# Performance work log

Hardware: AMD Instinct MI355X
Metric: run time of the kernel (lower is better)

## Reference

```python
import jax, jax.numpy as jnp
import numpy as np

B, T, C, HR = 8, 4096, 256, 4
N_LAYER, LAYER_ID = 12, 3
HID = HR * C


def _fancy_decay_first():
    # Faithful reproduction of VRWKV_SpatialMix._init_weights(init_mode='fancy')
    r01 = LAYER_ID / (N_LAYER - 1)
    h = np.arange(C, dtype=np.float32)
    decay = -5.0 + 8.0 * (h / (C - 1)) ** (0.7 + 1.3 * r01)
    zig = ((np.arange(1, C + 1) % 3) - 1).astype(np.float32) * 0.5
    first = np.float32(np.log(0.3)) + zig
    return jnp.asarray(decay, jnp.float32), jnp.asarray(first, jnp.float32)


def setup_inputs() -> dict:
    key = jax.random.key(0)
    ks = jax.random.split(key, 12)
    s = 0.02  # small weight scale keeps exp(k) well-conditioned
    decay, first = _fancy_decay_first()
    return {
        "x": jax.random.normal(ks[0], (B, T, C), jnp.float32),
        "Wk": jax.random.normal(ks[1], (C, C), jnp.float32) * s,
        "Wv": jax.random.normal(ks[2], (C, C), jnp.float32) * s,
        "Wr": jax.random.normal(ks[3], (C, C), jnp.float32) * s,
        "Wo": jax.random.normal(ks[4], (C, C), jnp.float32) * s,
        "Wk_ffn": jax.random.normal(ks[5], (C, HID), jnp.float32) * s,
        "Wv_ffn": jax.random.normal(ks[6], (HID, C), jnp.float32) * s,
        "Wr_ffn": jax.random.normal(ks[7], (C, C), jnp.float32) * s,
        "g1": 1.0 + 0.1 * jax.random.normal(ks[8], (C,), jnp.float32),
        "b1": 0.1 * jax.random.normal(ks[9], (C,), jnp.float32),
        "g2": 1.0 + 0.1 * jax.random.normal(ks[10], (C,), jnp.float32),
        "b2": 0.1 * jax.random.normal(ks[11], (C,), jnp.float32),
        "spatial_decay": decay,
        "spatial_first": first,
    }


def _ln(x, g, b):
    m = jnp.mean(x, axis=-1, keepdims=True)
    v = jnp.var(x, axis=-1, keepdims=True)
    return (x - m) * jax.lax.rsqrt(v + 1e-5) * g + b


def _wkv(w, u, k, v):
    # Numerically-stable log-space WKV recurrence (same math as wkv_cuda):
    # y_t = (sum_{i<t} e^{w*(t-1-i)+k_i} v_i + e^{u+k_t} v_t)
    #     / (sum_{i<t} e^{w*(t-1-i)+k_i}     + e^{u+k_t})
    # w,u: [C]; k,v: [B,T,C] -> y: [B,T,C]
    Bb, Tt, Cc = k.shape
    kT = jnp.swapaxes(k, 0, 1)  # [T,B,C]
    vT = jnp.swapaxes(v, 0, 1)

    def step(carry, kv):
        p, q, o = carry           # [B,C] num / den / running max exponent
        kt, vt = kv               # [B,C]
        no = jnp.maximum(o, u + kt)
        A = jnp.exp(o - no)
        E = jnp.exp(u + kt - no)
        y = (A * p + E * vt) / (A * q + E)
        no2 = jnp.maximum(w + o, kt)
        A2 = jnp.exp(w + o - no2)
        E2 = jnp.exp(kt - no2)
        return (A2 * p + E2 * vt, A2 * q + E2, no2), y

    init = (jnp.zeros((Bb, Cc), k.dtype),
            jnp.zeros((Bb, Cc), k.dtype),
            jnp.full((Bb, Cc), -1e38, k.dtype))
    _, yT = jax.lax.scan(step, init, (kT, vT))
    return jnp.swapaxes(yT, 0, 1)


def reference(x, Wk, Wv, Wr, Wo, Wk_ffn, Wv_ffn, Wr_ffn, g1, b1, g2, b2,
              spatial_decay, spatial_first):
    Tlen = x.shape[1]
    # --- SpatialMix (shift_pixel=0 -> xk=xv=xr=h, key_norm=False) ---
    h = _ln(x, g1, b1)
    k = h @ Wk
    v = h @ Wv
    sr = jax.nn.sigmoid(h @ Wr)
    y = _wkv(spatial_decay / Tlen, spatial_first / Tlen, k, v)
    x = x + (sr * y) @ Wo
    # --- ChannelMix (square-ReLU MLP, sigmoid receptance gate) ---
    h2 = _ln(x, g2, b2)
    kk = jnp.square(jax.nn.relu(h2 @ Wk_ffn))
    x = x + jax.nn.sigmoid(h2 @ Wr_ffn) * (kk @ Wv_ffn)
    return x
```

## Files before the change

### kernel.cpp

```cpp
#include <hip/hip_runtime.h>
#include <hip/hip_bf16.h>
#include <math.h>

#define TDIM 4096
#define CDIM 256
#define BDIM 8
#define NTOK (BDIM * TDIM)
#define HIDDIM 1024
#define NCHUNK 256
#define CHLEN 16

typedef float f32x4 __attribute__((ext_vector_type(4)));
typedef __bf16 bf16x8 __attribute__((ext_vector_type(8)));
typedef __bf16 bf16x4 __attribute__((ext_vector_type(4)));
typedef long long i64x2 __attribute__((ext_vector_type(2)));

#define GLDS16(gp, lp) __builtin_amdgcn_global_load_lds( \
    (const __attribute__((address_space(1))) void*)(gp), \
    (__attribute__((address_space(3))) void*)(lp), 16, 0, 0)

#define WAITCNT_VM8  0x0F78
#define WAITCNT_VM5  0x0F75
#define WAITCNT_VM4  0x0F74
#define WAITCNT_VM0  0x0F70

__device__ __forceinline__ float sigm(float v) { return 1.0f / (1.0f + __expf(-v)); }

__device__ __forceinline__ int permk(int k) {
  return (k & ~63) + (((k >> 3) & 3) << 4) + (((k >> 5) & 1) << 3) + (k & 7);
}

__global__ __launch_bounds__(256) void pack_weights(
    const float* __restrict__ Wk, const float* __restrict__ Wv,
    const float* __restrict__ Wr, const float* __restrict__ Wo,
    const float* __restrict__ Wkf, const float* __restrict__ Wvf,
    const float* __restrict__ Wrf,
    __bf16* __restrict__ WoT, unsigned char* __restrict__ Wkvr8,
    unsigned char* __restrict__ Wkfr8, unsigned char* __restrict__ Wvf8) {
  long long j = (long long)blockIdx.x * 256 + threadIdx.x;
  if (j < 49152) {
    const long long d = j * 4;
    const int n = (int)(d >> 8), k0 = (int)(d & 255);
    const float* src = (n < 256) ? Wk : (n < 512 ? Wv : Wr);
    const int nn = n & 255;
    int w = 0;
    w = __builtin_amdgcn_cvt_pk_fp8_f32(src[k0 * 256 + nn],
                                        src[(k0 + 1) * 256 + nn], w, false);
    w = __builtin_amdgcn_cvt_pk_fp8_f32(src[(k0 + 2) * 256 + nn],
                                        src[(k0 + 3) * 256 + nn], w, true);
    *(int*)&Wkvr8[(long long)n * 256 + permk(k0)] = w;
    return;
  }
  j -= 49152;
  if (j < 65536) { int n = (int)(j >> 8), k = (int)(j & 255);
    WoT[j] = (__bf16)Wo[k * 256 + n]; return; }
  j -= 65536;
  if (j < 81920) {
    const long long d = j * 4;
    const int n = (int)(d >> 8), k0 = (int)(d & 255);
    float v0, v1, v2, v3;
    if (n < 1024) {
      v0 = Wkf[(long long)k0 * 1024 + n];       v1 = Wkf[(long long)(k0 + 1) * 1024 + n];
      v2 = Wkf[(long long)(k0 + 2) * 1024 + n]; v3 = Wkf[(long long)(k0 + 3) * 1024 + n];
    } else {
      const int m = n - 1024;
      v0 = Wrf[k0 * 256 + m];       v1 = Wrf[(k0 + 1) * 256 + m];
      v2 = Wrf[(k0 + 2) * 256 + m]; v3 = Wrf[(k0 + 3) * 256 + m];
    }
    int w = 0;
    w = __builtin_amdgcn_cvt_pk_fp8_f32(v0, v1, w, false);
    w = __builtin_amdgcn_cvt_pk_fp8_f32(v2, v3, w, true);
    *(int*)&Wkfr8[(long long)n * 256 + permk(k0)] = w;
    return;
  }
  j -= 81920;
  if (j < 65536) {
    const long long d = j * 4;
    const int n = (int)(d >> 10), k0 = (int)(d & 1023);
    int w = 0;
    w = __builtin_amdgcn_cvt_pk_fp8_f32(Wvf[(long long)k0 * 256 + n],
                                        Wvf[(long long)(k0 + 1) * 256 + n], w, false);
    w = __builtin_amdgcn_cvt_pk_fp8_f32(Wvf[(long long)(k0 + 2) * 256 + n],
                                        Wvf[(long long)(k0 + 3) * 256 + n], w, true);
    *(int*)&Wvf8[(long long)n * 1024 + permk(k0)] = w;
    return;
  }
}

__global__ __launch_bounds__(256) void ln_kernel(
    const float* __restrict__ x, const float* __restrict__ gamma,
    const float* __restrict__ beta, unsigned char* __restrict__ h8) {
  const int wave = threadIdx.x >> 6, lane = threadIdx.x & 63;
  const long long row = (long long)blockIdx.x * 4 + wave;
  const long long base = row * CDIM + lane * 4;
  const f32x4 v = *(const f32x4*)&x[base];
  float s = v[0] + v[1] + v[2] + v[3];
  float s2 = v[0]*v[0] + v[1]*v[1] + v[2]*v[2] + v[3]*v[3];
  #pragma unroll
  for (int o = 1; o < 64; o <<= 1) { s += __shfl_xor(s, o); s2 += __shfl_xor(s2, o); }
  const float mean = s * (1.0f / CDIM);
  const float var = s2 * (1.0f / CDIM) - mean * mean;
  const float rstd = rsqrtf(var + 1e-5f);
  const f32x4 g4 = *(const f32x4*)&gamma[lane * 4];
  const f32x4 b4 = *(const f32x4*)&beta[lane * 4];
  float o0 = (v[0] - mean) * rstd * g4[0] + b4[0];
  float o1 = (v[1] - mean) * rstd * g4[1] + b4[1];
  float o2 = (v[2] - mean) * rstd * g4[2] + b4[2];
  float o3 = (v[3] - mean) * rstd * g4[3] + b4[3];
  int w = 0;
  w = __builtin_amdgcn_cvt_pk_fp8_f32(o0, o1, w, false);
  w = __builtin_amdgcn_cvt_pk_fp8_f32(o2, o3, w, true);
  *(int*)&h8[row * CDIM + permk(lane * 4)] = w;
}

template <int EPI, int NY>
__global__ __launch_bounds__(512, 4) void gemmF(
    const unsigned char* __restrict__ A8, const unsigned char* __restrict__ B8,
    __bf16* __restrict__ outH, __bf16* __restrict__ outH2,
    unsigned char* __restrict__ outC) {
  constexpr int NTILES = 256 * NY;
  constexpr int TPB = NTILES / 512;
  static_assert(NTILES % 512 == 0, "grid divisibility");
  __shared__ unsigned char sA[2][4 * 8192];

  const int tid = threadIdx.x;
  const int wave = tid >> 6, lane = tid & 63;
  const int quad = lane >> 4, mrow = lane & 15;
  const int wm = (wave & 1) * 64, wn = (wave >> 1) * 32;
  const int srow = lane >> 2;
  const int o16 = (lane & 3) * 16;
  const int t0 = blockIdx.x * TPB;

  auto issueA = [&](int t, int buf) {
    const long long bm = (long long)(t & 255) * 128;
    const int r0 = wave * 16;
    #pragma unroll
    for (int g = 0; g < 4; g++)
      GLDS16(A8 + (bm + r0 + srow) * 256 + g * 64 + o16,
             &sA[buf][g * 8192 + r0 * 64]);
  };

  i64x2 fb[2][4];
  auto loadB = [&](int y) {
    const long long bn = (long long)y * 128;
    #pragma unroll
    for (int nt = 0; nt < 2; nt++)
      #pragma unroll
      for (int g = 0; g < 4; g++)
        fb[nt][g] = *(const i64x2*)
            &B8[(bn + wn + nt * 16 + mrow) * 256 + g * 64 + quad * 16];
  };

  issueA(t0, 0);
  int prevy = -1;

  #pragma unroll 1
  for (int i = 0; i < TPB; i++) {
    const int t = t0 + i;
    const int y = t >> 8;
    const bool ych = (y != prevy);
    prevy = y;

    if (i == 0) __builtin_amdgcn_s_waitcnt(WAITCNT_VM0);
    else        __builtin_amdgcn_s_waitcnt(WAITCNT_VM8);
    __builtin_amdgcn_s_barrier();

    if (ych) loadB(y);
    if (i + 1 < TPB) issueA(t + 1, (i + 1) & 1);
    if (ych) __builtin_amdgcn_s_waitcnt(WAITCNT_VM8);

    f32x4 acc[4][2] = {};
    const int buf = i & 1;
    #pragma unroll
    for (int g = 0; g < 4; g++) {
      i64x2 fa[4];
      #pragma unroll
      for (int mt = 0; mt < 4; mt++)
        fa[mt] = *(const i64x2*)
            &sA[buf][g * 8192 + (wm + mt * 16 + mrow) * 64 + quad * 16];
      #pragma unroll
      for (int c = 0; c < 2; c++)
        #pragma unroll
        for (int mt = 0; mt < 4; mt++)
          #pragma unroll
          for (int nt = 0; nt < 2; nt++)
            acc[mt][nt] = __builtin_amdgcn_mfma_f32_16x16x32_fp8_fp8(
                fb[nt][g][c], fa[mt][c], acc[mt][nt], 0, 0, 0);
    }

    const long long bm = (long long)(t & 255) * 128;
    if (EPI == 0) {
      const int plane = y >> 1;
      __bf16* o = outH + (long long)plane * (32768LL * 256);
      const int cb = (y & 1) * 128 + wn + quad * 4;
      #pragma unroll
      for (int mt = 0; mt < 4; mt++) {
        const long long row = bm + wm + mt * 16 + mrow;
        #pragma unroll
        for (int nt = 0; nt < 2; nt++) {
          const f32x4 a = acc[mt][nt];
          bf16x4 v;
          if (plane == 2) {
            #pragma unroll
            for (int r = 0; r < 4; r++) v[r] = (__bf16)sigm(a[r]);
          } else {
            #pragma unroll
            for (int r = 0; r < 4; r++) v[r] = (__bf16)a[r];
          }
          *(bf16x4*)&o[row * 256 + cb + nt * 16] = v;
        }
      }
    } else {
      if (y < 8) {
        const int cb = y * 128 + wn + quad * 4;
        #pragma unroll
        for (int mt = 0; mt < 4; mt++) {
          const long long row = bm + wm + mt * 16 + mrow;
          #pragma unroll
          for (int nt = 0; nt < 2; nt++) {
            const f32x4 a = acc[mt][nt];
            float q0 = a[0] > 0.0f ? a[0] : 0.0f;
            float q1 = a[1] > 0.0f ? a[1] : 0.0f;
            float q2 = a[2] > 0.0f ? a[2] : 0.0f;
            float q3 = a[3] > 0.0f ? a[3] : 0.0f;
            int w = 0;
            w = __builtin_amdgcn_cvt_pk_fp8_f32(q0 * q0, q1 * q1, w, false);
            w = __builtin_amdgcn_cvt_pk_fp8_f32(q2 * q2, q3 * q3, w, true);
            *(int*)&outC[row * 1024 + permk(cb + nt * 16)] = w;
          }
        }
      } else {
        const int cb = (y - 8) * 128 + wn + quad * 4;
        #pragma unroll
        for (int mt = 0; mt < 4; mt++) {
          const long long row = bm + wm + mt * 16 + mrow;
          #pragma unroll
          for (int nt = 0; nt < 2; nt++) {
            const f32x4 a = acc[mt][nt];
            bf16x4 v;
            #pragma unroll
            for (int r = 0; r < 4; r++) v[r] = (__bf16)sigm(a[r]);
            *(bf16x4*)&outH2[row * 256 + cb + nt * 16] = v;
          }
        }
      }
    }
  }
}

template <int K, int EPI>
__global__ __launch_bounds__(256, 3) void gemm9(
    const unsigned char* __restrict__ A8, const unsigned char* __restrict__ B8,
    int M, __bf16* __restrict__ outH, __bf16* __restrict__ outH2,
    unsigned char* __restrict__ outC,
    float* __restrict__ outF, const __bf16* __restrict__ srcH,
    const __bf16* __restrict__ gate) {
  constexpr int NIT = K / 64;
  __shared__ unsigned char sA[3][128 * 64];
  __shared__ unsigned char sB[3][128 * 64];
  const int tid = threadIdx.x;
  const int wave = tid >> 6, lane = tid & 63;
  const int quad = lane >> 4, mrow = lane & 15;
  const long long bm = (long long)blockIdx.x * 128;
  const long long bn = (long long)blockIdx.y * 128;
  const int wm = (wave & 1) * 64, wn = (wave >> 1) * 64;
  const int srow = lane >> 2;
  const int o16 = (lane & 3) * 16;

  auto issue = [&](int g) {
    const int buf = g % 3;
    const long long k0 = (long long)g * 64;
    const int a0 = wave * 32;
    GLDS16(A8 + (bm + a0 + srow) * (long long)K + k0 + o16, &sA[buf][a0 * 64]);
    GLDS16(A8 + (bm + a0 + 16 + srow) * (long long)K + k0 + o16, &sA[buf][(a0 + 16) * 64]);
    GLDS16(B8 + (bn + a0 + srow) * (long long)K + k0 + o16, &sB[buf][a0 * 64]);
    GLDS16(B8 + (bn + a0 + 16 + srow) * (long long)K + k0 + o16, &sB[buf][(a0 + 16) * 64]);
  };

  f32x4 acc[4][4] = {};
  issue(0);
  if (NIT > 1) issue(1);

  auto compute = [&](int g) {
    const int buf = g % 3;
    i64x2 fa[4], fb[4];
    #pragma unroll
    for (int mt = 0; mt < 4; mt++)
      fa[mt] = *(const i64x2*)&sA[buf][(wm + mt * 16 + mrow) * 64 + quad * 16];
    #pragma unroll
    for (int nt = 0; nt < 4; nt++)
      fb[nt] = *(const i64x2*)&sB[buf][(wn + nt * 16 + mrow) * 64 + quad * 16];
    #pragma unroll
    for (int c = 0; c < 2; c++)
      #pragma unroll
      for (int mt = 0; mt < 4; mt++)
        #pragma unroll
        for (int nt = 0; nt < 4; nt++)
          acc[mt][nt] = __builtin_amdgcn_mfma_f32_16x16x32_fp8_fp8(
              fb[nt][c], fa[mt][c], acc[mt][nt], 0, 0, 0);
  };

  #pragma unroll 1
  for (int g = 0; g < NIT; g++) {
    if (g == NIT - 1) {
      __builtin_amdgcn_s_waitcnt(WAITCNT_VM0);
    } else {
      __builtin_amdgcn_s_waitcnt(WAITCNT_VM4);
    }
    __builtin_amdgcn_s_barrier();
    if (g + 2 < NIT) issue(g + 2);
    compute(g);
  }

  #pragma unroll
  for (int mt = 0; mt < 4; mt++) {
    #pragma unroll
    for (int nt = 0; nt < 4; nt++) {
      const long long row = bm + wm + mt * 16 + mrow;
      const long long colb = bn + wn + nt * 16 + quad * 4;
      const f32x4 a = acc[mt][nt];
      if (EPI == 0) {
        const int plane = blockIdx.y >> 1;
        __bf16* o = outH + (long long)plane * ((long long)M * 256);
        const long long c2 = colb & 255;
        bf16x4 v;
        if (plane == 2) {
          #pragma unroll
          for (int r = 0; r < 4; r++) v[r] = (__bf16)sigm(a[r]);
        } else {
          #pragma unroll
          for (int r = 0; r < 4; r++) v[r] = (__bf16)a[r];
        }
        *(bf16x4*)&o[row * 256 + c2] = v;
      } else if (EPI == 2) {
        if (blockIdx.y < 8) {
          float t0 = a[0] > 0.0f ? a[0] : 0.0f;
          float t1 = a[1] > 0.0f ? a[1] : 0.0f;
          float t2 = a[2] > 0.0f ? a[2] : 0.0f;
          float t3 = a[3] > 0.0f ? a[3] : 0.0f;
          int w = 0;
          w = __builtin_amdgcn_cvt_pk_fp8_f32(t0 * t0, t1 * t1, w, false);
          w = __builtin_amdgcn_cvt_pk_fp8_f32(t2 * t2, t3 * t3, w, true);
          *(int*)&outC[row * 1024 + permk((int)colb)] = w;
        } else {
          bf16x4 v;
          #pragma unroll
          for (int r = 0; r < 4; r++) v[r] = (__bf16)sigm(a[r]);
          *(bf16x4*)&outH2[row * 256 + (colb - 1024)] = v;
        }
      } else {
        const long long idx = row * 256 + colb;
        const bf16x4 s4 = *(const bf16x4*)&srcH[idx];
        const bf16x4 g4 = *(const bf16x4*)&gate[idx];
        f32x4 v;
        #pragma unroll
        for (int r = 0; r < 4; r++) v[r] = (float)s4[r] + (float)g4[r] * a[r];
        *(f32x4*)&outF[idx] = v;
      }
    }
  }
}

__global__ __launch_bounds__(256, 2) void gemm7(
    const __bf16* __restrict__ A, const __bf16* __restrict__ Bt,
    const float* __restrict__ x,
    const float* __restrict__ gammaP, const float* __restrict__ betaP,
    __bf16* __restrict__ x1h, unsigned char* __restrict__ h28) {
  constexpr int K = 256;
  __shared__ __bf16 sA[3][64 * 32];
  __shared__ __bf16 sB[3][256 * 32];
  __shared__ float redS[4][64], redQ[4][64];

  const int tid = threadIdx.x;
  const int wave = tid >> 6, lane = tid & 63;
  const int quad = lane >> 4, mrow = lane & 15;
  const long long bm = (long long)blockIdx.x * 64;
  const int wn = wave * 64;
  const int lrow = lane >> 2;
  const int lk = (lane & 3) * 8;

  auto issue = [&](int g) {
    const int buf = g % 3;
    const long long k0 = (long long)g * 32;
    GLDS16(A + (bm + wave * 16 + lrow) * (long long)K + k0 + lk,
           &sA[buf][(wave * 16) * 32]);
    #pragma unroll
    for (int bc = 0; bc < 4; bc++) {
      const int r0 = wave * 64 + bc * 16;
      GLDS16(Bt + (r0 + lrow) * (long long)K + k0 + lk, &sB[buf][r0 * 32]);
    }
  };

  f32x4 acc[4][4] = {};

  auto compute = [&](int g) {
    const int buf = g % 3;
    bf16x8 fa[4], fb[4];
    #pragma unroll
    for (int mt = 0; mt < 4; mt++)
      fa[mt] = *(const bf16x8*)&sA[buf][(mt * 16 + mrow) * 32 + quad * 8];
    #pragma unroll
    for (int nt = 0; nt < 4; nt++)
      fb[nt] = *(const bf16x8*)&sB[buf][(wn + nt * 16 + mrow) * 32 + quad * 8];
    #pragma unroll
    for (int mt = 0; mt < 4; mt++)
      #pragma unroll
      for (int nt = 0; nt < 4; nt++)
        acc[mt][nt] = __builtin_amdgcn_mfma_f32_16x16x32_bf16(fb[nt], fa[mt], acc[mt][nt], 0, 0, 0);
  };

  issue(0);
  issue(1);
  #pragma unroll 1
  for (int g = 0; g < 8; g++) {
    if (g == 7) {
      __builtin_amdgcn_s_waitcnt(WAITCNT_VM0);
    } else {
      __builtin_amdgcn_s_waitcnt(WAITCNT_VM5);
    }
    __builtin_amdgcn_s_barrier();
    if (g + 2 < 8) issue(g + 2);
    compute(g);
  }

  float sum[4] = {0, 0, 0, 0}, sq[4] = {0, 0, 0, 0};
  #pragma unroll
  for (int mt = 0; mt < 4; mt++) {
    #pragma unroll
    for (int nt = 0; nt < 4; nt++) {
      const long long row = bm + mt * 16 + mrow;
      const long long colb = wn + nt * 16 + quad * 4;
      acc[mt][nt] += *(const f32x4*)&x[row * 256 + colb];
      #pragma unroll
      for (int r = 0; r < 4; r++) {
        sum[mt] += acc[mt][nt][r];
        sq[mt] += acc[mt][nt][r] * acc[mt][nt][r];
      }
    }
  }
  #pragma unroll
  for (int mt = 0; mt < 4; mt++) {
    sum[mt] += __shfl_xor(sum[mt], 16); sq[mt] += __shfl_xor(sq[mt], 16);
    sum[mt] += __shfl_xor(sum[mt], 32); sq[mt] += __shfl_xor(sq[mt], 32);
  }
  if (quad == 0) {
    #pragma unroll
    for (int mt = 0; mt < 4; mt++) {
      redS[wave][mt * 16 + mrow] = sum[mt];
      redQ[wave][mt * 16 + mrow] = sq[mt];
    }
  }
  __syncthreads();
  #pragma unroll
  for (int mt = 0; mt < 4; mt++) {
    const int rb = mt * 16 + mrow;
    const float ts = redS[0][rb] + redS[1][rb] + redS[2][rb] + redS[3][rb];
    const float tq = redQ[0][rb] + redQ[1][rb] + redQ[2][rb] + redQ[3][rb];
    const float mean = ts * (1.0f / 256.0f);
    const float rstd = rsqrtf(tq * (1.0f / 256.0f) - mean * mean + 1e-5f);
    const long long row = bm + rb;
    #pragma unroll
    for (int nt = 0; nt < 4; nt++) {
      const long long colb = wn + nt * 16 + quad * 4;
      const f32x4 g4 = *(const f32x4*)&gammaP[colb];
      const f32x4 b4 = *(const f32x4*)&betaP[colb];
      bf16x4 xo;
      const float t0 = acc[mt][nt][0], t1 = acc[mt][nt][1];
      const float t2 = acc[mt][nt][2], t3 = acc[mt][nt][3];
      xo[0] = (__bf16)t0; xo[1] = (__bf16)t1; xo[2] = (__bf16)t2; xo[3] = (__bf16)t3;
      const float h0 = (t0 - mean) * rstd * g4[0] + b4[0];
      const float h1 = (t1 - mean) * rstd * g4[1] + b4[1];
      const float h2v = (t2 - mean) * rstd * g4[2] + b4[2];
      const float h3 = (t3 - mean) * rstd * g4[3] + b4[3];
      *(bf16x4*)&x1h[row * 256 + colb] = xo;
      int w = 0;
      w = __builtin_amdgcn_cvt_pk_fp8_f32(h0, h1, w, false);
      w = __builtin_amdgcn_cvt_pk_fp8_f32(h2v, h3, w, true);
      *(int*)&h28[row * 256 + permk((int)colb)] = w;
    }
  }
}

__global__ __launch_bounds__(256) void wkv_phase1(
    const __bf16* __restrict__ ka, const __bf16* __restrict__ va,
    const float* __restrict__ decay,
    float* __restrict__ Sloc, float* __restrict__ Zloc) {
  const int wave = threadIdx.x >> 6, lane = threadIdx.x & 63;
  const int gi = blockIdx.x * 4 + wave;
  const int b = gi >> 8, chunk = gi & (NCHUNK - 1);
  const int c0 = lane * 4;
  const f32x4 w4 = *(const f32x4*)&decay[c0];
  f32x4 ew;
  #pragma unroll
  for (int r = 0; r < 4; r++) ew[r] = __expf(w4[r] * (1.0f / TDIM));
  f32x4 S = {0,0,0,0}, Z = {0,0,0,0};
  long long base = ((long long)b * TDIM + (long long)chunk * CHLEN) * 256 + c0;
  #pragma unroll 4
  for (int t = 0; t < CHLEN; t++) {
    const bf16x4 k4 = *(const bf16x4*)&ka[base + (long long)t * 256];
    const bf16x4 v4 = *(const bf16x4*)&va[base + (long long)t * 256];
    #pragma unroll
    for (int r = 0; r < 4; r++) {
      const float ek = __expf((float)k4[r]);
      S[r] = ew[r] * S[r] + ek * (float)v4[r];
      Z[r] = ew[r] * Z[r] + ek;
    }
  }
  const long long o = (long long)gi * 256 + c0;
  *(f32x4*)&Sloc[o] = S;
  *(f32x4*)&Zloc[o] = Z;
}

__global__ __launch_bounds__(256) void wkv_phase2(
    const float* __restrict__ Sloc, const float* __restrict__ Zloc,
    const float* __restrict__ decay,
    float* __restrict__ Sstart, float* __restrict__ Zstart) {
  const int idx = blockIdx.x * 256 + threadIdx.x;
  const int c = idx & 255;
  const int b = idx >> 8;
  const float w = decay[c] * (1.0f / TDIM);
  const float ewL = __expf(w * (float)CHLEN);
  float S = 0.0f, Z = 0.0f;
  for (int j = 0; j < NCHUNK; j++) {
    const long long o = ((long long)b * NCHUNK + j) * 256 + c;
    Sstart[o] = S;
    Zstart[o] = Z;
    S = ewL * S + Sloc[o];
    Z = ewL * Z + Zloc[o];
  }
}

__global__ __launch_bounds__(256) void wkv_phase3(
    const __bf16* __restrict__ ka, const __bf16* __restrict__ va,
    const __bf16* __restrict__ ra,
    const float* __restrict__ decay, const float* __restrict__ first,
    const float* __restrict__ Sstart, const float* __restrict__ Zstart,
    __bf16* __restrict__ a2) {
  const int wave = threadIdx.x >> 6, lane = threadIdx.x & 63;
  const int gi = blockIdx.x * 4 + wave;
  const int b = gi >> 8, chunk = gi & (NCHUNK - 1);
  const int c0 = lane * 4;
  const f32x4 w4 = *(const f32x4*)&decay[c0];
  const f32x4 u4 = *(const f32x4*)&first[c0];
  f32x4 ew, eu;
  #pragma unroll
  for (int r = 0; r < 4; r++) {
    ew[r] = __expf(w4[r] * (1.0f / TDIM));
    eu[r] = __expf(u4[r] * (1.0f / TDIM));
  }
  const long long so = (long long)gi * 256 + c0;
  f32x4 S = *(const f32x4*)&Sstart[so];
  f32x4 Z = *(const f32x4*)&Zstart[so];
  long long base = ((long long)b * TDIM + (long long)chunk * CHLEN) * 256 + c0;
  #pragma unroll 2
  for (int t = 0; t < CHLEN; t++) {
    const long long p = base + (long long)t * 256;
    const bf16x4 k4 = *(const bf16x4*)&ka[p];
    const bf16x4 v4 = *(const bf16x4*)&va[p];
    const bf16x4 r4 = *(const bf16x4*)&ra[p];
    bf16x4 o;
    #pragma unroll
    for (int r = 0; r < 4; r++) {
      const float ek = __expf((float)k4[r]);
      const float E = eu[r] * ek;
      const float y = (S[r] + E * (float)v4[r]) / (Z[r] + E);
      o[r] = (__bf16)((float)r4[r] * y);
      S[r] = ew[r] * S[r] + ek * (float)v4[r];
      Z[r] = ew[r] * Z[r] + ek;
    }
    *(bf16x4*)&a2[p] = o;
  }
}

extern "C" void kernel_launch(void* const* d_in, const int* in_sizes, int n_in,
                              void* d_out, int out_size, void* d_ws, size_t ws_size,
                              hipStream_t stream) {
  const float* x     = (const float*)d_in[0];
  const float* Wk    = (const float*)d_in[1];
  const float* Wv    = (const float*)d_in[2];
  const float* Wr    = (const float*)d_in[3];
  const float* Wo    = (const float*)d_in[4];
  const float* Wkf   = (const float*)d_in[5];
  const float* Wvf   = (const float*)d_in[6];
  const float* Wrf   = (const float*)d_in[7];
  const float* g1    = (const float*)d_in[8];
  const float* b1    = (const float*)d_in[9];
  const float* g2    = (const float*)d_in[10];
  const float* b2    = (const float*)d_in[11];
  const float* decay = (const float*)d_in[12];
  const float* first = (const float*)d_in[13];
  float* out = (float*)d_out;
  char* ws = (char*)d_ws;

  __bf16* ka     = (__bf16*)(ws + 0);
  __bf16* va     = (__bf16*)(ws + 16777216LL);
  __bf16* ra     = (__bf16*)(ws + 33554432LL);
  __bf16* a2     = (__bf16*)(ws + 50331648LL);
  __bf16* g2buf  = (__bf16*)(ws + 50331648LL);
  unsigned char* h8  = (unsigned char*)(ws + 67108864LL);
  unsigned char* h28 = (unsigned char*)(ws + 67108864LL);
  __bf16* x1h    = (__bf16*)(ws + 83886080LL);
  unsigned char* kk8 = (unsigned char*)(ws + 100663296LL);
  float*  Sloc   = (float*)(ws + 134217728LL);
  float*  Zloc   = (float*)(ws + 137363456LL);
  float*  Sstart = (float*)(ws + 140509184LL);
  float*  Zstart = (float*)(ws + 143654912LL);
  __bf16* WoT    = (__bf16*)(ws + 167772160LL);
  unsigned char* Wkvr8 = (unsigned char*)(ws + 167903232LL);
  unsigned char* Wkfr8 = (unsigned char*)(ws + 168099840LL);
  unsigned char* Wvf8  = (unsigned char*)(ws + 168427520LL);

  pack_weights<<<1024, 256, 0, stream>>>(Wk, Wv, Wr, Wo, Wkf, Wvf, Wrf,
                                         WoT, Wkvr8, Wkfr8, Wvf8);

  ln_kernel<<<NTOK / 4, 256, 0, stream>>>(x, g1, b1, h8);
  gemmF<0, 6><<<512, 512, 0, stream>>>(h8, Wkvr8, ka, nullptr, nullptr);
  wkv_phase1<<<BDIM * NCHUNK / 4, 256, 0, stream>>>(ka, va, decay, Sloc, Zloc);
  wkv_phase2<<<BDIM, 256, 0, stream>>>(Sloc, Zloc, decay, Sstart, Zstart);
  wkv_phase3<<<BDIM * NCHUNK / 4, 256, 0, stream>>>(ka, va, ra, decay, first,
                                                    Sstart, Zstart, a2);
  gemm7<<<NTOK / 64, 256, 0, stream>>>(a2, WoT, x, g2, b2, x1h, h28);

  gemmF<2, 10><<<512, 512, 0, stream>>>(h28, Wkfr8, nullptr, g2buf, kk8);
  gemm9<1024, 3><<<dim3(NTOK / 128, 2), 256, 0, stream>>>(
      kk8, Wvf8, NTOK, nullptr, nullptr, nullptr, out, x1h, g2buf);
}
```

Before: 255.7 us.

## Parallelize WKV chunk scan with wave shuffles, precompute exp(k), add MFMA priority

The sequential cross-chunk scan in wkv_phase2, which ran on only 8 blocks with one thread per channel, is replaced by a wave-level parallel prefix scan using shuffles, launched across many more blocks. Chunks are halved to length 8 so there are twice as many. exp(k) is computed once in the GEMM epilogue and stored, so phases 1 and 3 no longer recompute it. s_setprio is raised around the MFMA loops, and one redundant waitcnt is removed. Storing exp(k) in bf16 instead of k could change precision, and removing the waitcnt risks a race on B loads.

```diff
diff --git a/kernel.cpp b/kernel.cpp
--- a/kernel.cpp
+++ b/kernel.cpp
@@ -7,8 +7,8 @@
 #define BDIM 8
 #define NTOK (BDIM * TDIM)
 #define HIDDIM 1024
-#define NCHUNK 256
-#define CHLEN 16
+#define NCHUNK 512
+#define CHLEN 8
 
 typedef float f32x4 __attribute__((ext_vector_type(4)));
 typedef __bf16 bf16x8 __attribute__((ext_vector_type(8)));
@@ -167,10 +167,10 @@
 
     if (ych) loadB(y);
     if (i + 1 < TPB) issueA(t + 1, (i + 1) & 1);
-    if (ych) __builtin_amdgcn_s_waitcnt(WAITCNT_VM8);
 
     f32x4 acc[4][2] = {};
     const int buf = i & 1;
+    __builtin_amdgcn_s_setprio(1);
     #pragma unroll
     for (int g = 0; g < 4; g++) {
       i64x2 fa[4];
@@ -187,6 +187,7 @@
             acc[mt][nt] = __builtin_amdgcn_mfma_f32_16x16x32_fp8_fp8(
                 fb[nt][g][c], fa[mt][c], acc[mt][nt], 0, 0, 0);
     }
+    __builtin_amdgcn_s_setprio(0);
 
     const long long bm = (long long)(t & 255) * 128;
     if (EPI == 0) {
@@ -203,6 +204,9 @@
           if (plane == 2) {
             #pragma unroll
             for (int r = 0; r < 4; r++) v[r] = (__bf16)sigm(a[r]);
+          } else if (plane == 0) {
+            #pragma unroll
+            for (int r = 0; r < 4; r++) v[r] = (__bf16)__expf(a[r]);
           } else {
             #pragma unroll
             for (int r = 0; r < 4; r++) v[r] = (__bf16)a[r];
@@ -290,6 +294,7 @@
     #pragma unroll
     for (int nt = 0; nt < 4; nt++)
       fb[nt] = *(const i64x2*)&sB[buf][(wn + nt * 16 + mrow) * 64 + quad * 16];
+    __builtin_amdgcn_s_setprio(1);
     #pragma unroll
     for (int c = 0; c < 2; c++)
       #pragma unroll
@@ -298,6 +303,7 @@
         for (int nt = 0; nt < 4; nt++)
           acc[mt][nt] = __builtin_amdgcn_mfma_f32_16x16x32_fp8_fp8(
               fb[nt][c], fa[mt][c], acc[mt][nt], 0, 0, 0);
+    __builtin_amdgcn_s_setprio(0);
   };
 
   #pragma unroll 1
@@ -402,11 +408,13 @@
     #pragma unroll
     for (int nt = 0; nt < 4; nt++)
       fb[nt] = *(const bf16x8*)&sB[buf][(wn + nt * 16 + mrow) * 32 + quad * 8];
+    __builtin_amdgcn_s_setprio(1);
     #pragma unroll
     for (int mt = 0; mt < 4; mt++)
       #pragma unroll
       for (int nt = 0; nt < 4; nt++)
         acc[mt][nt] = __builtin_amdgcn_mfma_f32_16x16x32_bf16(fb[nt], fa[mt], acc[mt][nt], 0, 0, 0);
+    __builtin_amdgcn_s_setprio(0);
   };
 
   issue(0);
@@ -487,7 +495,7 @@
     float* __restrict__ Sloc, float* __restrict__ Zloc) {
   const int wave = threadIdx.x >> 6, lane = threadIdx.x & 63;
   const int gi = blockIdx.x * 4 + wave;
-  const int b = gi >> 8, chunk = gi & (NCHUNK - 1);
+  const int b = gi / NCHUNK, chunk = gi & (NCHUNK - 1);
   const int c0 = lane * 4;
   const f32x4 w4 = *(const f32x4*)&decay[c0];
   f32x4 ew;
@@ -495,13 +503,13 @@
   for (int r = 0; r < 4; r++) ew[r] = __expf(w4[r] * (1.0f / TDIM));
   f32x4 S = {0,0,0,0}, Z = {0,0,0,0};
   long long base = ((long long)b * TDIM + (long long)chunk * CHLEN) * 256 + c0;
-  #pragma unroll 4
+  #pragma unroll
   for (int t = 0; t < CHLEN; t++) {
     const bf16x4 k4 = *(const bf16x4*)&ka[base + (long long)t * 256];
     const bf16x4 v4 = *(const bf16x4*)&va[base + (long long)t * 256];
     #pragma unroll
     for (int r = 0; r < 4; r++) {
-      const float ek = __expf((float)k4[r]);
+      const float ek = (float)k4[r];
       S[r] = ew[r] * S[r] + ek * (float)v4[r];
       Z[r] = ew[r] * Z[r] + ek;
     }
@@ -515,18 +523,40 @@
     const float* __restrict__ Sloc, const float* __restrict__ Zloc,
     const float* __restrict__ decay,
     float* __restrict__ Sstart, float* __restrict__ Zstart) {
-  const int idx = blockIdx.x * 256 + threadIdx.x;
-  const int c = idx & 255;
-  const int b = idx >> 8;
+  const int wave = threadIdx.x >> 6, lane = threadIdx.x & 63;
+  const int idx = blockIdx.x * 4 + wave;
+  const int b = idx >> 8, c = idx & 255;
   const float w = decay[c] * (1.0f / TDIM);
   const float ewL = __expf(w * (float)CHLEN);
-  float S = 0.0f, Z = 0.0f;
-  for (int j = 0; j < NCHUNK; j++) {
-    const long long o = ((long long)b * NCHUNK + j) * 256 + c;
-    Sstart[o] = S;
-    Zstart[o] = Z;
-    S = ewL * S + Sloc[o];
-    Z = ewL * Z + Zloc[o];
+  const float a8  = __expf(w * (float)(CHLEN * 8));
+  constexpr int CPL = NCHUNK / 64;
+  float Sv[CPL], Zv[CPL];
+  const long long base = ((long long)b * NCHUNK + lane * CPL) * 256 + c;
+  #pragma unroll
+  for (int i = 0; i < CPL; i++) {
+    Sv[i] = Sloc[base + (long long)i * 256];
+    Zv[i] = Zloc[base + (long long)i * 256];
+  }
+  float s = 0.0f, z = 0.0f;
+  #pragma unroll
+  for (int i = 0; i < CPL; i++) { s = ewL * s + Sv[i]; z = ewL * z + Zv[i]; }
+  float f = a8;
+  #pragma unroll
+  for (int off = 1; off < 64; off <<= 1) {
+    const float ps = __shfl_up(s, off);
+    const float pz = __shfl_up(z, off);
+    if (lane >= off) { s += f * ps; z += f * pz; }
+    f *= f;
+  }
+  float cs = __shfl_up(s, 1);
+  float cz = __shfl_up(z, 1);
+  if (lane == 0) { cs = 0.0f; cz = 0.0f; }
+  #pragma unroll
+  for (int i = 0; i < CPL; i++) {
+    Sstart[base + (long long)i * 256] = cs;
+    Zstart[base + (long long)i * 256] = cz;
+    cs = ewL * cs + Sv[i];
+    cz = ewL * cz + Zv[i];
   }
 }
 
@@ -538,7 +568,7 @@
     __bf16* __restrict__ a2) {
   const int wave = threadIdx.x >> 6, lane = threadIdx.x & 63;
   const int gi = blockIdx.x * 4 + wave;
-  const int b = gi >> 8, chunk = gi & (NCHUNK - 1);
+  const int b = gi / NCHUNK, chunk = gi & (NCHUNK - 1);
   const int c0 = lane * 4;
   const f32x4 w4 = *(const f32x4*)&decay[c0];
   const f32x4 u4 = *(const f32x4*)&first[c0];
@@ -552,7 +582,7 @@
   f32x4 S = *(const f32x4*)&Sstart[so];
   f32x4 Z = *(const f32x4*)&Zstart[so];
   long long base = ((long long)b * TDIM + (long long)chunk * CHLEN) * 256 + c0;
-  #pragma unroll 2
+  #pragma unroll 4
   for (int t = 0; t < CHLEN; t++) {
     const long long p = base + (long long)t * 256;
     const bf16x4 k4 = *(const bf16x4*)&ka[p];
@@ -561,7 +591,7 @@
     bf16x4 o;
     #pragma unroll
     for (int r = 0; r < 4; r++) {
-      const float ek = __expf((float)k4[r]);
+      const float ek = (float)k4[r];
       const float E = eu[r] * ek;
       const float y = (S[r] + E * (float)v4[r]) / (Z[r] + E);
       o[r] = (__bf16)((float)r4[r] * y);
@@ -602,9 +632,9 @@
   __bf16* x1h    = (__bf16*)(ws + 83886080LL);
   unsigned char* kk8 = (unsigned char*)(ws + 100663296LL);
   float*  Sloc   = (float*)(ws + 134217728LL);
-  float*  Zloc   = (float*)(ws + 137363456LL);
-  float*  Sstart = (float*)(ws + 140509184LL);
-  float*  Zstart = (float*)(ws + 143654912LL);
+  float*  Zloc   = (float*)(ws + 138412032LL);
+  float*  Sstart = (float*)(ws + 142606336LL);
+  float*  Zstart = (float*)(ws + 146800640LL);
   __bf16* WoT    = (__bf16*)(ws + 167772160LL);
   unsigned char* Wkvr8 = (unsigned char*)(ws + 167903232LL);
   unsigned char* Wkfr8 = (unsigned char*)(ws + 168099840LL);
@@ -616,7 +646,7 @@
   ln_kernel<<<NTOK / 4, 256, 0, stream>>>(x, g1, b1, h8);
   gemmF<0, 6><<<512, 512, 0, stream>>>(h8, Wkvr8, ka, nullptr, nullptr);
   wkv_phase1<<<BDIM * NCHUNK / 4, 256, 0, stream>>>(ka, va, decay, Sloc, Zloc);
-  wkv_phase2<<<BDIM, 256, 0, stream>>>(Sloc, Zloc, decay, Sstart, Zstart);
+  wkv_phase2<<<BDIM * CDIM / 4, 256, 0, stream>>>(Sloc, Zloc, decay, Sstart, Zstart);
   wkv_phase3<<<BDIM * NCHUNK / 4, 256, 0, stream>>>(ka, va, ra, decay, first,
                                                     Sstart, Zstart, a2);
   gemm7<<<NTOK / 64, 256, 0, stream>>>(a2, WoT, x, g2, b2, x1h, h28);
```

New measurement: 266.3 us. 1.04x slower.

## Stage gemmF epilogue through LDS for coalesced stores and merge LN into prep kernel

Applied to the files above, without the earlier changes.

The gemmF epilogues now write results into the just-consumed A buffer in LDS with an XOR swizzle, fence, then emit full 16-byte coalesced global stores per row instead of scattered 8-byte/4-byte writes. The waitcnt scheme is relaxed (VM4/VM2 instead of VM8 plus a post-loadB wait), which changes how many loads stay in flight. The layernorm kernel is folded into the weight-packing kernel as extra blocks, removing one launch. It adds two barriers per tile and reuses the A buffer for staging, which risks races or pipeline stalls. Dead EPI branches in gemm9 are removed.

```diff
diff --git a/kernel.cpp b/kernel.cpp
--- a/kernel.cpp
+++ b/kernel.cpp
@@ -22,7 +22,16 @@
 #define WAITCNT_VM8  0x0F78
 #define WAITCNT_VM5  0x0F75
 #define WAITCNT_VM4  0x0F74
+#define WAITCNT_VM2  0x0F72
 #define WAITCNT_VM0  0x0F70
+#define WAITCNT_LGKM0 0xC07F
+
+#define STAGE_FENCE() do { \
+    __builtin_amdgcn_sched_barrier(0); \
+    __builtin_amdgcn_s_waitcnt(WAITCNT_LGKM0); \
+    __builtin_amdgcn_s_barrier(); \
+    __builtin_amdgcn_sched_barrier(0); \
+  } while (0)
 
 __device__ __forceinline__ float sigm(float v) { return 1.0f / (1.0f + __expf(-v)); }
 
@@ -30,13 +39,39 @@
   return (k & ~63) + (((k >> 3) & 3) << 4) + (((k >> 5) & 1) << 3) + (k & 7);
 }
 
-__global__ __launch_bounds__(256) void pack_weights(
+__global__ __launch_bounds__(256) void prep(
     const float* __restrict__ Wk, const float* __restrict__ Wv,
     const float* __restrict__ Wr, const float* __restrict__ Wo,
     const float* __restrict__ Wkf, const float* __restrict__ Wvf,
     const float* __restrict__ Wrf,
     __bf16* __restrict__ WoT, unsigned char* __restrict__ Wkvr8,
-    unsigned char* __restrict__ Wkfr8, unsigned char* __restrict__ Wvf8) {
+    unsigned char* __restrict__ Wkfr8, unsigned char* __restrict__ Wvf8,
+    const float* __restrict__ x, const float* __restrict__ gamma,
+    const float* __restrict__ beta, unsigned char* __restrict__ h8) {
+  if (blockIdx.x >= 1024) {
+    const int wave = threadIdx.x >> 6, lane = threadIdx.x & 63;
+    const long long row = (long long)(blockIdx.x - 1024) * 4 + wave;
+    const long long base = row * CDIM + lane * 4;
+    const f32x4 v = *(const f32x4*)&x[base];
+    float s = v[0] + v[1] + v[2] + v[3];
+    float s2 = v[0]*v[0] + v[1]*v[1] + v[2]*v[2] + v[3]*v[3];
+    #pragma unroll
+    for (int o = 1; o < 64; o <<= 1) { s += __shfl_xor(s, o); s2 += __shfl_xor(s2, o); }
+    const float mean = s * (1.0f / CDIM);
+    const float var = s2 * (1.0f / CDIM) - mean * mean;
+    const float rstd = rsqrtf(var + 1e-5f);
+    const f32x4 g4 = *(const f32x4*)&gamma[lane * 4];
+    const f32x4 b4 = *(const f32x4*)&beta[lane * 4];
+    float o0 = (v[0] - mean) * rstd * g4[0] + b4[0];
+    float o1 = (v[1] - mean) * rstd * g4[1] + b4[1];
+    float o2 = (v[2] - mean) * rstd * g4[2] + b4[2];
+    float o3 = (v[3] - mean) * rstd * g4[3] + b4[3];
+    int w = 0;
+    w = __builtin_amdgcn_cvt_pk_fp8_f32(o0, o1, w, false);
+    w = __builtin_amdgcn_cvt_pk_fp8_f32(o2, o3, w, true);
+    *(int*)&h8[row * CDIM + permk(lane * 4)] = w;
+    return;
+  }
   long long j = (long long)blockIdx.x * 256 + threadIdx.x;
   if (j < 49152) {
     const long long d = j * 4;
@@ -87,32 +122,6 @@
   }
 }
 
-__global__ __launch_bounds__(256) void ln_kernel(
-    const float* __restrict__ x, const float* __restrict__ gamma,
-    const float* __restrict__ beta, unsigned char* __restrict__ h8) {
-  const int wave = threadIdx.x >> 6, lane = threadIdx.x & 63;
-  const long long row = (long long)blockIdx.x * 4 + wave;
-  const long long base = row * CDIM + lane * 4;
-  const f32x4 v = *(const f32x4*)&x[base];
-  float s = v[0] + v[1] + v[2] + v[3];
-  float s2 = v[0]*v[0] + v[1]*v[1] + v[2]*v[2] + v[3]*v[3];
-  #pragma unroll
-  for (int o = 1; o < 64; o <<= 1) { s += __shfl_xor(s, o); s2 += __shfl_xor(s2, o); }
-  const float mean = s * (1.0f / CDIM);
-  const float var = s2 * (1.0f / CDIM) - mean * mean;
-  const float rstd = rsqrtf(var + 1e-5f);
-  const f32x4 g4 = *(const f32x4*)&gamma[lane * 4];
-  const f32x4 b4 = *(const f32x4*)&beta[lane * 4];
-  float o0 = (v[0] - mean) * rstd * g4[0] + b4[0];
-  float o1 = (v[1] - mean) * rstd * g4[1] + b4[1];
-  float o2 = (v[2] - mean) * rstd * g4[2] + b4[2];
-  float o3 = (v[3] - mean) * rstd * g4[3] + b4[3];
-  int w = 0;
-  w = __builtin_amdgcn_cvt_pk_fp8_f32(o0, o1, w, false);
-  w = __builtin_amdgcn_cvt_pk_fp8_f32(o2, o3, w, true);
-  *(int*)&h8[row * CDIM + permk(lane * 4)] = w;
-}
-
 template <int EPI, int NY>
 __global__ __launch_bounds__(512, 4) void gemmF(
     const unsigned char* __restrict__ A8, const unsigned char* __restrict__ B8,
@@ -161,13 +170,13 @@
     const bool ych = (y != prevy);
     prevy = y;
 
-    if (i == 0) __builtin_amdgcn_s_waitcnt(WAITCNT_VM0);
-    else        __builtin_amdgcn_s_waitcnt(WAITCNT_VM8);
+    if (i == 0)          __builtin_amdgcn_s_waitcnt(WAITCNT_VM0);
+    else if (EPI == 0)   __builtin_amdgcn_s_waitcnt(WAITCNT_VM4);
+    else                 __builtin_amdgcn_s_waitcnt(WAITCNT_VM2);
     __builtin_amdgcn_s_barrier();
 
     if (ych) loadB(y);
     if (i + 1 < TPB) issueA(t + 1, (i + 1) & 1);
-    if (ych) __builtin_amdgcn_s_waitcnt(WAITCNT_VM8);
 
     f32x4 acc[4][2] = {};
     const int buf = i & 1;
@@ -188,14 +197,16 @@
                 fb[nt][g][c], fa[mt][c], acc[mt][nt], 0, 0, 0);
     }
 
+    __builtin_amdgcn_s_barrier();
+    unsigned char* stg = &sA[buf][0];
     const long long bm = (long long)(t & 255) * 128;
+
     if (EPI == 0) {
       const int plane = y >> 1;
-      __bf16* o = outH + (long long)plane * (32768LL * 256);
-      const int cb = (y & 1) * 128 + wn + quad * 4;
       #pragma unroll
       for (int mt = 0; mt < 4; mt++) {
-        const long long row = bm + wm + mt * 16 + mrow;
+        const int row = wm + mt * 16 + mrow;
+        const int swz = (row & 7) << 4;
         #pragma unroll
         for (int nt = 0; nt < 2; nt++) {
           const f32x4 a = acc[mt][nt];
@@ -207,15 +218,26 @@
             #pragma unroll
             for (int r = 0; r < 4; r++) v[r] = (__bf16)a[r];
           }
-          *(bf16x4*)&o[row * 256 + cb + nt * 16] = v;
+          const int cb2 = (wn + nt * 16 + quad * 4) * 2;
+          *(bf16x4*)&stg[row * 256 + (cb2 ^ swz)] = v;
         }
+      }
+      STAGE_FENCE();
+      char* ob = (char*)(outH + (long long)plane * (32768LL * 256));
+      const int row = tid >> 2, qb = (tid & 3) * 64;
+      const int swz = (row & 7) << 4;
+      const long long gb = (bm + row) * 512 + (long long)(y & 1) * 256 + qb;
+      #pragma unroll
+      for (int c = 0; c < 4; c++) {
+        const i64x2 d = *(const i64x2*)&stg[row * 256 + ((qb + c * 16) ^ swz)];
+        *(i64x2*)&ob[gb + c * 16] = d;
       }
     } else {
       if (y < 8) {
-        const int cb = y * 128 + wn + quad * 4;
         #pragma unroll
         for (int mt = 0; mt < 4; mt++) {
-          const long long row = bm + wm + mt * 16 + mrow;
+          const int row = wm + mt * 16 + mrow;
+          const int swz = (row & 7) << 4;
           #pragma unroll
           for (int nt = 0; nt < 2; nt++) {
             const f32x4 a = acc[mt][nt];
@@ -226,22 +248,43 @@
             int w = 0;
             w = __builtin_amdgcn_cvt_pk_fp8_f32(q0 * q0, q1 * q1, w, false);
             w = __builtin_amdgcn_cvt_pk_fp8_f32(q2 * q2, q3 * q3, w, true);
-            *(int*)&outC[row * 1024 + permk(cb + nt * 16)] = w;
+            const int cbl = wn + nt * 16 + quad * 4;
+            *(int*)&stg[row * 128 + (permk(cbl) ^ swz)] = w;
           }
         }
+        STAGE_FENCE();
+        const int row = tid >> 2, sb = (tid & 3) * 32;
+        const int swz = (row & 7) << 4;
+        const long long gb = (bm + row) * 1024 + (long long)y * 128 + sb;
+        #pragma unroll
+        for (int c = 0; c < 2; c++) {
+          const i64x2 d = *(const i64x2*)&stg[row * 128 + ((sb + c * 16) ^ swz)];
+          *(i64x2*)&outC[gb + c * 16] = d;
+        }
       } else {
-        const int cb = (y - 8) * 128 + wn + quad * 4;
         #pragma unroll
         for (int mt = 0; mt < 4; mt++) {
-          const long long row = bm + wm + mt * 16 + mrow;
+          const int row = wm + mt * 16 + mrow;
+          const int swz = (row & 7) << 4;
           #pragma unroll
           for (int nt = 0; nt < 2; nt++) {
             const f32x4 a = acc[mt][nt];
             bf16x4 v;
             #pragma unroll
             for (int r = 0; r < 4; r++) v[r] = (__bf16)sigm(a[r]);
-            *(bf16x4*)&outH2[row * 256 + cb + nt * 16] = v;
+            const int cb2 = (wn + nt * 16 + quad * 4) * 2;
+            *(bf16x4*)&stg[row * 256 + (cb2 ^ swz)] = v;
           }
+        }
+        STAGE_FENCE();
+        char* ob = (char*)outH2;
+        const int row = tid >> 2, qb = (tid & 3) * 64;
+        const int swz = (row & 7) << 4;
+        const long long gb = (bm + row) * 512 + (long long)(y - 8) * 256 + qb;
+        #pragma unroll
+        for (int c = 0; c < 4; c++) {
+          const i64x2 d = *(const i64x2*)&stg[row * 256 + ((qb + c * 16) ^ swz)];
+          *(i64x2*)&ob[gb + c * 16] = d;
         }
       }
     }
@@ -319,44 +362,13 @@
       const long long row = bm + wm + mt * 16 + mrow;
       const long long colb = bn + wn + nt * 16 + quad * 4;
       const f32x4 a = acc[mt][nt];
-      if (EPI == 0) {
-        const int plane = blockIdx.y >> 1;
-        __bf16* o = outH + (long long)plane * ((long long)M * 256);
-        const long long c2 = colb & 255;
-        bf16x4 v;
-        if (plane == 2) {
-          #pragma unroll
-          for (int r = 0; r < 4; r++) v[r] = (__bf16)sigm(a[r]);
-        } else {
-          #pragma unroll
-          for (int r = 0; r < 4; r++) v[r] = (__bf16)a[r];
-        }
-        *(bf16x4*)&o[row * 256 + c2] = v;
-      } else if (EPI == 2) {
-        if (blockIdx.y < 8) {
-          float t0 = a[0] > 0.0f ? a[0] : 0.0f;
-          float t1 = a[1] > 0.0f ? a[1] : 0.0f;
-          float t2 = a[2] > 0.0f ? a[2] : 0.0f;
-          float t3 = a[3] > 0.0f ? a[3] : 0.0f;
-          int w = 0;
-          w = __builtin_amdgcn_cvt_pk_fp8_f32(t0 * t0, t1 * t1, w, false);
-          w = __builtin_amdgcn_cvt_pk_fp8_f32(t2 * t2, t3 * t3, w, true);
-          *(int*)&outC[row * 1024 + permk((int)colb)] = w;
-        } else {
-          bf16x4 v;
-          #pragma unroll
-          for (int r = 0; r < 4; r++) v[r] = (__bf16)sigm(a[r]);
-          *(bf16x4*)&outH2[row * 256 + (colb - 1024)] = v;
-        }
-      } else {
-        const long long idx = row * 256 + colb;
-        const bf16x4 s4 = *(const bf16x4*)&srcH[idx];
-        const bf16x4 g4 = *(const bf16x4*)&gate[idx];
-        f32x4 v;
-        #pragma unroll
-        for (int r = 0; r < 4; r++) v[r] = (float)s4[r] + (float)g4[r] * a[r];
-        *(f32x4*)&outF[idx] = v;
-      }
+      const long long idx = row * 256 + colb;
+      const bf16x4 s4 = *(const bf16x4*)&srcH[idx];
+      const bf16x4 g4 = *(const bf16x4*)&gate[idx];
+      f32x4 v;
+      #pragma unroll
+      for (int r = 0; r < 4; r++) v[r] = (float)s4[r] + (float)g4[r] * a[r];
+      *(f32x4*)&outF[idx] = v;
     }
   }
 }
@@ -610,10 +622,10 @@
   unsigned char* Wkfr8 = (unsigned char*)(ws + 168099840LL);
   unsigned char* Wvf8  = (unsigned char*)(ws + 168427520LL);
 
-  pack_weights<<<1024, 256, 0, stream>>>(Wk, Wv, Wr, Wo, Wkf, Wvf, Wrf,
-                                         WoT, Wkvr8, Wkfr8, Wvf8);
-
-  ln_kernel<<<NTOK / 4, 256, 0, stream>>>(x, g1, b1, h8);
+  prep<<<1024 + NTOK / 4, 256, 0, stream>>>(
+      Wk, Wv, Wr, Wo, Wkf, Wvf, Wrf, WoT, Wkvr8, Wkfr8, Wvf8,
+      x, g1, b1, h8);
+
   gemmF<0, 6><<<512, 512, 0, stream>>>(h8, Wkvr8, ka, nullptr, nullptr);
   wkv_phase1<<<BDIM * NCHUNK / 4, 256, 0, stream>>>(ka, va, decay, Sloc, Zloc);
   wkv_phase2<<<BDIM, 256, 0, stream>>>(Sloc, Zloc, decay, Sstart, Zstart);
```

Result: no change. 256.1 us (+0.1%).
